# Kernel tuning notes

Measured on AMD Instinct MI355X. Metric: run time of the kernel, lower is better.

## Reference

```python
import jax, jax.numpy as jnp
import numpy as np

D = 1024
H = 16
DH = D // H
L = 128  # max_pos_len
B = 4
T = 1024
SCALE = float(np.sqrt(D / H))


def setup_inputs() -> dict:
    key = jax.random.key(0)
    ks = jax.random.split(key, 9)
    x_q = jax.random.normal(ks[0], (B, T, D), dtype=jnp.float32)
    x_k = jax.random.normal(ks[1], (B, T, D), dtype=jnp.float32)
    x_v = jax.random.normal(ks[2], (B, T, D), dtype=jnp.float32)
    mask = jax.random.randint(ks[3], (B, 1, 1, T), 0, 2) == 1  # bool, True = masked
    Wq = jax.random.normal(ks[4], (D, D), dtype=jnp.float32) * 0.02
    Wk = jax.random.normal(ks[5], (D, D), dtype=jnp.float32) * 0.02
    Wv = jax.random.normal(ks[6], (D, D), dtype=jnp.float32) * 0.02
    Wo = jax.random.normal(ks[7], (D, D), dtype=jnp.float32) * 0.02
    pos_emb = jax.random.normal(ks[8], (2 * L + 1, DH), dtype=jnp.float32)
    return {"x_q": x_q, "x_k": x_k, "x_v": x_v, "mask": mask,
            "Wq": Wq, "Wk": Wk, "Wv": Wv, "Wo": Wo, "pos_emb": pos_emb}


def reference(x_q, x_k, x_v, mask, Wq, Wk, Wv, Wo, pos_emb):
    # nn.Linear(bias=False): y = x @ W.T
    def split_heads(x):  # (B,T,D) -> (B,H,T,DH)
        return x.reshape(B, -1, H, DH).transpose(0, 2, 1, 3)

    Q = split_heads(x_q @ Wq.T)
    K = split_heads(x_k @ Wk.T)
    V = split_heads(x_v @ Wv.T)

    logits = jnp.einsum('bhqd,bhkd->bhqk', Q, K)

    # arrange_char_pos_embedding: indices[q,k] = clamp(k-q, -L, L) + L
    rel = jnp.clip(jnp.arange(T)[None, :] - jnp.arange(T)[:, None], -L, L) + L
    arranged_pos = pos_emb[rel]  # (T_Q, T_K, DH)
    pos_logits = jnp.einsum('bhqd,qkd->bhqk', Q, arranged_pos)

    logits = (logits + pos_logits) / SCALE
    logits = jnp.where(mask, -jnp.inf, logits)  # mask broadcasts (B,1,1,T)
    attn = jax.nn.softmax(logits, axis=-1)  # dropout p=0.0 -> identity

    combined = jnp.einsum('bhqk,bhkd->bhqd', attn, V)
    heads_concat = combined.transpose(0, 2, 1, 3).reshape(B, -1, D)
    return heads_concat @ Wo.T
```

## Files before the change

kernel.cpp:

```cpp
#include <hip/hip_runtime.h>
#include <hip/hip_bf16.h>
#include <stdint.h>

typedef __attribute__((ext_vector_type(8))) short short8;
typedef __attribute__((ext_vector_type(4))) float f32x4;

__device__ __forceinline__ uint16_t f2bf(float f) {
    union { float f; uint32_t u; } v; v.f = f;
    uint32_t r = v.u + 0x7FFF + ((v.u >> 16) & 1);
    return (uint16_t)(r >> 16);
}
__device__ __forceinline__ float bf2f(uint16_t u) {
    union { uint32_t u; float f; } v; v.u = ((uint32_t)u) << 16;
    return v.f;
}

template<int F32>
__device__ __forceinline__ uint4 load8(const void* p, size_t off) {
    if (F32) {
        const float* f = (const float*)p + off;
        float4 f0 = *(const float4*)f;
        float4 f1 = *(const float4*)(f + 4);
        uint4 r;
        r.x = (uint32_t)f2bf(f0.x) | ((uint32_t)f2bf(f0.y) << 16);
        r.y = (uint32_t)f2bf(f0.z) | ((uint32_t)f2bf(f0.w) << 16);
        r.z = (uint32_t)f2bf(f1.x) | ((uint32_t)f2bf(f1.y) << 16);
        r.w = (uint32_t)f2bf(f1.z) | ((uint32_t)f2bf(f1.w) << 16);
        return r;
    } else {
        return *(const uint4*)((const uint16_t*)p + off);
    }
}

#define GLDS(gp, lp) __builtin_amdgcn_global_load_lds( \
    (const __attribute__((address_space(1))) void*)(gp), \
    (__attribute__((address_space(3))) void*)(lp), 16, 0, 0)

struct CvtSeg { const float* s; uint16_t* d; int n8; };
struct CvtArgs { CvtSeg seg[9]; int nseg; const void* mraw; int* mcanon; };

__global__ __launch_bounds__(256) void cvt_bf16(CvtArgs a)
{
    if (blockIdx.x == 0) {
        __shared__ int flags[3];
        const uint32_t* w = (const uint32_t*)a.mraw;
        const uint8_t* b8 = (const uint8_t*)a.mraw;
        const int t = threadIdx.x;
        if (t < 3) flags[t] = 0;
        __syncthreads();
        int fbyte = 0, ff32 = 0, fodd = 0;
        for (int i = t; i < 1024; i += 256) {
            uint32_t v = w[i];
            if (v != 0u && v != 1u && v != 0x3F800000u) fbyte = 1;
            if (v == 0x3F800000u) ff32 = 1;
            if ((i & 1) && v != 0u) fodd = 1;
        }
        if (fbyte) atomicOr(&flags[0], 1);
        if (ff32)  atomicOr(&flags[1], 1);
        if (fodd)  atomicOr(&flags[2], 1);
        __syncthreads();
        int mode;
        if (flags[0]) mode = 1;
        else if (flags[1]) mode = 0;
        else if (!flags[2]) mode = 2;
        else mode = 0;
        for (int k = t; k < 4096; k += 256) {
            int val;
            if (mode == 1)      val = (b8[k] != 0);
            else if (mode == 2) val = (w[2 * k] != 0u);
            else                val = (w[k] != 0u);
            a.mcanon[k] = val;
        }
    }
    const int tid = blockIdx.x * 256 + threadIdx.x;
    const int stride = gridDim.x * 256;
    for (int s = 0; s < a.nseg; ++s) {
        const float* src = a.seg[s].s;
        uint16_t* dst = a.seg[s].d;
        const int n8 = a.seg[s].n8;
        if (src) {
            for (int i = tid; i < n8; i += stride)
                *(uint4*)(dst + (size_t)i * 8) = load8<1>(src, (size_t)i * 8);
        } else {
            const uint4 z = {0u, 0u, 0u, 0u};
            for (int i = tid; i < n8; i += stride)
                *(uint4*)(dst + (size_t)i * 8) = z;
        }
    }
}

__global__ __launch_bounds__(256) void gemm128_qkv(
    const uint16_t* __restrict__ xq, const uint16_t* __restrict__ xk, const uint16_t* __restrict__ xv,
    const uint16_t* __restrict__ Wq, const uint16_t* __restrict__ Wk, const uint16_t* __restrict__ Wv,
    uint16_t* __restrict__ Qh, uint16_t* __restrict__ Khd, uint16_t* __restrict__ Vt)
{
    __shared__ alignas(16) uint16_t As[2][128 * 32];
    __shared__ alignas(16) uint16_t Bs[2][128 * 32];

    const int z = blockIdx.z;
    const uint16_t* A = (z == 0) ? xq : (z == 1) ? xk : xv;
    const uint16_t* B = (z == 0) ? Wq : (z == 1) ? Wk : Wv;
    uint16_t* C = (z == 0) ? Qh : (z == 1) ? Khd : Vt;
    const int cm = (z == 2) ? 2 : 1;
    const int bm = blockIdx.x, bn = blockIdx.y;
    const int K = 1024;

    const int t = threadIdx.x;
    const int lane = t & 63, wave = t >> 6;
    const int lrow = lane & 15, quad = lane >> 4;
    const int wr = (wave >> 1) * 64, wc = (wave & 1) * 64;
    const int g_row = wave * 16 + (lane >> 2);
    const int g_col = (lane & 3) * 8;

    const f32x4 fz = {0.f, 0.f, 0.f, 0.f};
    f32x4 acc[4][4];
#pragma unroll
    for (int i = 0; i < 4; ++i)
#pragma unroll
        for (int j = 0; j < 4; ++j) acc[i][j] = fz;

    for (int k0 = 0; k0 < K; k0 += 64) {
        __syncthreads();
#pragma unroll
        for (int kh = 0; kh < 2; ++kh) {
            const int kk = k0 + kh * 32;
            GLDS(A + (size_t)(bm * 128 + g_row) * K + kk + g_col,      As[kh] + wave * 512);
            GLDS(A + (size_t)(bm * 128 + g_row + 64) * K + kk + g_col, As[kh] + wave * 512 + 2048);
            GLDS(B + (size_t)(bn * 128 + g_row) * K + kk + g_col,      Bs[kh] + wave * 512);
            GLDS(B + (size_t)(bn * 128 + g_row + 64) * K + kk + g_col, Bs[kh] + wave * 512 + 2048);
        }
        __syncthreads();

#pragma unroll
        for (int kh = 0; kh < 2; ++kh) {
            short8 a[4], b[4];
#pragma unroll
            for (int i = 0; i < 4; ++i)
                a[i] = *(const short8*)(As[kh] + (wr + i * 16 + lrow) * 32 + quad * 8);
#pragma unroll
            for (int j = 0; j < 4; ++j)
                b[j] = *(const short8*)(Bs[kh] + (wc + j * 16 + lrow) * 32 + quad * 8);
#pragma unroll
            for (int i = 0; i < 4; ++i)
#pragma unroll
                for (int j = 0; j < 4; ++j)
                    acc[i][j] = __builtin_amdgcn_mfma_f32_16x16x32_bf16(a[i], b[j], acc[i][j], 0, 0, 0);
        }
    }

    if (cm == 2) {
        __syncthreads();
        uint16_t* scr = As[0] + wave * 1024;
#pragma unroll
        for (int i = 0; i < 4; ++i)
#pragma unroll
            for (int j = 0; j < 4; ++j) {
                uint2 pk;
                pk.x = (uint32_t)f2bf(acc[i][j][0]) | ((uint32_t)f2bf(acc[i][j][1]) << 16);
                pk.y = (uint32_t)f2bf(acc[i][j][2]) | ((uint32_t)f2bf(acc[i][j][3]) << 16);
                *(uint2*)(scr + lrow * 16 + quad * 4) = pk;
                if (lane < 32) {
                    int n = lane >> 1, m8 = (lane & 1) * 8;
                    short8 vv = *(const short8*)(scr + n * 16 + m8);
                    int ng = bn * 128 + wc + j * 16 + n;
                    int hh = ng >> 6, d = ng & 63;
                    int mg = bm * 128 + wr + i * 16;
                    int bb = mg >> 10, tl = (mg & 1023) + m8;
                    *(short8*)(C + ((((size_t)bb * 16 + hh) * 64 + d) * 1024 + tl)) = vv;
                }
            }
        return;
    }

#pragma unroll
    for (int i = 0; i < 4; ++i)
#pragma unroll
        for (int j = 0; j < 4; ++j)
#pragma unroll
            for (int r = 0; r < 4; ++r) {
                int m = bm * 128 + wr + i * 16 + quad * 4 + r;
                int n = bn * 128 + wc + j * 16 + lrow;
                int bb = m >> 10, tt = m & 1023, hh = n >> 6, d = n & 63;
                C[(((size_t)bb * 16 + hh) * 1024 + tt) * 64 + d] = f2bf(acc[i][j][r]);
            }
}

__global__ __launch_bounds__(256) void gemm_out(
    const uint16_t* __restrict__ A, const uint16_t* __restrict__ B,
    float* __restrict__ C, int M, int N, int K)
{
    __shared__ alignas(16) uint16_t As[2][64 * 32];
    __shared__ alignas(16) uint16_t Bs[2][128 * 32];

    const int t = threadIdx.x;
    const int lane = t & 63, wave = t >> 6;
    const int lrow = lane & 15, quad = lane >> 4;
    const int wr = (wave >> 1) * 32, wc = (wave & 1) * 64;
    const int g_row = wave * 16 + (lane >> 2);
    const int g_col = (lane & 3) * 8;
    const int bm = blockIdx.x, bn = blockIdx.y;

    const f32x4 fz = {0.f, 0.f, 0.f, 0.f};
    f32x4 acc[2][4];
#pragma unroll
    for (int i = 0; i < 2; ++i)
#pragma unroll
        for (int j = 0; j < 4; ++j) acc[i][j] = fz;

    for (int k0 = 0; k0 < K; k0 += 64) {
        __syncthreads();
#pragma unroll
        for (int kh = 0; kh < 2; ++kh) {
            const int kk = k0 + kh * 32;
            GLDS(A + (size_t)(bm * 64 + g_row) * K + kk + g_col,       As[kh] + wave * 512);
            GLDS(B + (size_t)(bn * 128 + g_row) * K + kk + g_col,      Bs[kh] + wave * 512);
            GLDS(B + (size_t)(bn * 128 + g_row + 64) * K + kk + g_col, Bs[kh] + wave * 512 + 2048);
        }
        __syncthreads();

#pragma unroll
        for (int kh = 0; kh < 2; ++kh) {
            short8 a[2], b[4];
#pragma unroll
            for (int i = 0; i < 2; ++i)
                a[i] = *(const short8*)(As[kh] + (wr + i * 16 + lrow) * 32 + quad * 8);
#pragma unroll
            for (int j = 0; j < 4; ++j)
                b[j] = *(const short8*)(Bs[kh] + (wc + j * 16 + lrow) * 32 + quad * 8);
#pragma unroll
            for (int i = 0; i < 2; ++i)
#pragma unroll
                for (int j = 0; j < 4; ++j)
                    acc[i][j] = __builtin_amdgcn_mfma_f32_16x16x32_bf16(a[i], b[j], acc[i][j], 0, 0, 0);
        }
    }

#pragma unroll
    for (int i = 0; i < 2; ++i)
#pragma unroll
        for (int j = 0; j < 4; ++j)
#pragma unroll
            for (int r = 0; r < 4; ++r) {
                int m = bm * 64 + wr + i * 16 + quad * 4 + r;
                int n = bn * 128 + wc + j * 16 + lrow;
                C[(size_t)m * N + n] = acc[i][j][r];
            }
}

__global__ __launch_bounds__(256) void flash_attn(
    const uint16_t* __restrict__ Qh, const uint16_t* __restrict__ Kh,
    const uint16_t* __restrict__ Vt, const uint16_t* __restrict__ pos,
    const int* __restrict__ mask, uint16_t* __restrict__ comb)
{
    const int blk = blockIdx.x;
    const int jj = blk >> 3;
    const int bh = (blk & 7) * 8 + (jj >> 4);
    const int qt = jj & 15;
    const int b = bh >> 4;
    const int h = bh & 15;
    const int t = threadIdx.x;
    const int lane = t & 63;
    const int wave = t >> 6;
    const int lrow = lane & 15;
    const int quad = lane >> 4;
    const int qb = qt * 64 + wave * 16;

    __shared__ alignas(16) uint16_t Ks[2][4096];
    __shared__ alignas(16) uint16_t Vs[2][4096];
    __shared__ alignas(16) uint16_t Qpos_l[64][274];
    __shared__ alignas(16) uint16_t Pl[4][16][72];

    const uint16_t* Kp = Kh + (size_t)bh * 65536;
    const uint16_t* Vp = Vt + (size_t)bh * 65536;
    const int* mk = mask + b * 1024;

    const int sg_r = lane >> 2;
    const int sg_c = (lane & 3) * 8;
    const int hw = wave >> 1;
    const int gw = (wave & 1) * 2;

#pragma unroll
    for (int gg = 0; gg < 2; ++gg) {
        int g = gw + gg;
        GLDS(Kp + (size_t)(g * 16 + sg_r) * 64 + hw * 32 + sg_c, &Ks[0][hw * 2048 + g * 512]);
        GLDS(Vp + (size_t)(g * 16 + sg_r) * 1024 + hw * 32 + sg_c, &Vs[0][hw * 2048 + g * 512]);
    }

    const uint16_t* Qp = Qh + ((size_t)bh * 1024 + qb) * 64;
    short8 aq0 = *(const short8*)(Qp + (size_t)lrow * 64 + quad * 8);
    short8 aq1 = *(const short8*)(Qp + (size_t)lrow * 64 + 32 + quad * 8);

    const f32x4 fz = {0.f, 0.f, 0.f, 0.f};

#pragma unroll 4
    for (int nt = 0; nt < 17; ++nt) {
        short8 pb0 = *(const short8*)(pos + (size_t)(nt * 16 + lrow) * 64 + quad * 8);
        short8 pb1 = *(const short8*)(pos + (size_t)(nt * 16 + lrow) * 64 + 32 + quad * 8);
        f32x4 c = __builtin_amdgcn_mfma_f32_16x16x32_bf16(aq0, pb0, fz, 0, 0, 0);
        c = __builtin_amdgcn_mfma_f32_16x16x32_bf16(aq1, pb1, c, 0, 0, 0);
#pragma unroll
        for (int r = 0; r < 4; ++r)
            Qpos_l[wave * 16 + quad * 4 + r][nt * 16 + lrow] = f2bf(c[r]);
    }

    float pcl[4], pch[4];
#pragma unroll
    for (int r = 0; r < 4; ++r) {
        int ql = wave * 16 + quad * 4 + r;
        pcl[r] = bf2f(Qpos_l[ql][0])   * 0.125f;
        pch[r] = bf2f(Qpos_l[ql][256]) * 0.125f;
    }

    f32x4 o[4] = {fz, fz, fz, fz};
    float lsum[4] = {0.f, 0.f, 0.f, 0.f};

    for (int kb = 0; kb < 1024; kb += 64) {
        const int cur = (kb >> 6) & 1;
        __syncthreads();
        if (kb + 64 < 1024) {
            const int nxt = cur ^ 1;
#pragma unroll
            for (int gg = 0; gg < 2; ++gg) {
                int g = gw + gg;
                GLDS(Kp + (size_t)(kb + 64 + g * 16 + sg_r) * 64 + hw * 32 + sg_c,
                     &Ks[nxt][hw * 2048 + g * 512]);
                GLDS(Vp + (size_t)(g * 16 + sg_r) * 1024 + kb + 64 + hw * 32 + sg_c,
                     &Vs[nxt][hw * 2048 + g * 512]);
            }
        }
        const uint16_t* Kc = Ks[cur];
        const uint16_t* Vc = Vs[cur];

        f32x4 s[4];
#pragma unroll
        for (int j = 0; j < 4; ++j) {
            short8 k0 = *(const short8*)(Kc + (j * 16 + lrow) * 32 + quad * 8);
            short8 k1 = *(const short8*)(Kc + 2048 + (j * 16 + lrow) * 32 + quad * 8);
            s[j] = __builtin_amdgcn_mfma_f32_16x16x32_bf16(aq0, k0, fz, 0, 0, 0);
            s[j] = __builtin_amdgcn_mfma_f32_16x16x32_bf16(aq1, k1, s[j], 0, 0, 0);
        }

        const int diff = kb - qb;
        if (diff <= -192 || diff >= 144) {
            const bool low = (diff <= -192);
#pragma unroll
            for (int j = 0; j < 4; ++j) {
                const int key = kb + j * 16 + lrow;
                const bool m = (mk[key] != 0);
#pragma unroll
                for (int r = 0; r < 4; ++r) {
                    float pc = low ? pcl[r] : pch[r];
                    float e = m ? 0.f : __expf(__builtin_fmaf(s[j][r], 0.125f, pc));
                    lsum[r] += e;
                    Pl[wave][quad * 4 + r][j * 16 + lrow] = f2bf(e);
                }
            }
        } else {
#pragma unroll
            for (int j = 0; j < 4; ++j) {
                const int key = kb + j * 16 + lrow;
                const bool m = (mk[key] != 0);
#pragma unroll
                for (int r = 0; r < 4; ++r) {
                    int q = qb + quad * 4 + r;
                    int ql = q & 63;
                    int rel = min(max(key - q, -128), 128) + 128;
                    float p = bf2f(Qpos_l[ql][rel]);
                    float e = m ? 0.f : __expf((s[j][r] + p) * 0.125f);
                    lsum[r] += e;
                    Pl[wave][quad * 4 + r][j * 16 + lrow] = f2bf(e);
                }
            }
        }
        short8 ap0 = *(const short8*)(&Pl[wave][lrow][quad * 8]);
        short8 ap1 = *(const short8*)(&Pl[wave][lrow][32 + quad * 8]);

#pragma unroll
        for (int dt = 0; dt < 4; ++dt) {
            short8 v0 = *(const short8*)(Vc + (dt * 16 + lrow) * 32 + quad * 8);
            short8 v1 = *(const short8*)(Vc + 2048 + (dt * 16 + lrow) * 32 + quad * 8);
            o[dt] = __builtin_amdgcn_mfma_f32_16x16x32_bf16(ap0, v0, o[dt], 0, 0, 0);
            o[dt] = __builtin_amdgcn_mfma_f32_16x16x32_bf16(ap1, v1, o[dt], 0, 0, 0);
        }
    }

#pragma unroll
    for (int off = 1; off < 16; off <<= 1)
#pragma unroll
        for (int r = 0; r < 4; ++r)
            lsum[r] += __shfl_xor(lsum[r], off);

    float inv[4];
#pragma unroll
    for (int r = 0; r < 4; ++r) inv[r] = 1.0f / lsum[r];

#pragma unroll
    for (int dt = 0; dt < 4; ++dt)
#pragma unroll
        for (int r = 0; r < 4; ++r) {
            size_t row = (size_t)b * 1024 + qb + quad * 4 + r;
            size_t col = (size_t)h * 64 + dt * 16 + lrow;
            comb[row * 1024 + col] = f2bf(o[dt][r] * inv[r]);
        }
}

extern "C" void kernel_launch(void* const* d_in, const int* in_sizes, int n_in,
                              void* d_out, int out_size, void* d_ws, size_t ws_size,
                              hipStream_t stream)
{
    const float* x_q = (const float*)d_in[0];
    const float* x_k = (const float*)d_in[1];
    const float* x_v = (const float*)d_in[2];
    const void*  msk = d_in[3];
    const float* Wq  = (const float*)d_in[4];
    const float* Wk  = (const float*)d_in[5];
    const float* Wv  = (const float*)d_in[6];
    const float* Wo  = (const float*)d_in[7];
    const float* pos = (const float*)d_in[8];

    char* ws = (char*)d_ws;
    const size_t MB = 1u << 20;
    uint16_t* Qh   = (uint16_t*)(ws);
    uint16_t* Khd  = (uint16_t*)(ws + 8 * MB);
    uint16_t* Vt   = (uint16_t*)(ws + 16 * MB);
    uint16_t* xqb  = (uint16_t*)(ws + 24 * MB);
    uint16_t* xkb  = (uint16_t*)(ws + 32 * MB);
    uint16_t* xvb  = (uint16_t*)(ws + 40 * MB);
    uint16_t* Wqb  = (uint16_t*)(ws + 48 * MB);
    uint16_t* Wkb  = (uint16_t*)(ws + 50 * MB);
    uint16_t* Wvb  = (uint16_t*)(ws + 52 * MB);
    uint16_t* Wob  = (uint16_t*)(ws + 54 * MB);
    uint16_t* posb = (uint16_t*)(ws + 56 * MB);
    int*      canon = (int*)(ws + 56 * MB + 65536);
    uint16_t* comb = xqb;

    CvtArgs ca{};
    int ns = 0;
    ca.seg[ns++] = {x_q, xqb, 524288};
    ca.seg[ns++] = {x_k, xkb, 524288};
    ca.seg[ns++] = {x_v, xvb, 524288};
    ca.seg[ns++] = {Wq, Wqb, 131072};
    ca.seg[ns++] = {Wk, Wkb, 131072};
    ca.seg[ns++] = {Wv, Wvb, 131072};
    ca.seg[ns++] = {Wo, Wob, 131072};
    ca.seg[ns++] = {pos, posb, 2056};
    ca.seg[ns++] = {nullptr, posb + 16448, 120};
    ca.nseg = ns;
    ca.mraw = msk;
    ca.mcanon = canon;
    cvt_bf16<<<dim3(512), dim3(256), 0, stream>>>(ca);

    gemm128_qkv<<<dim3(32, 8, 3), dim3(256), 0, stream>>>(
        xqb, xkb, xvb, Wqb, Wkb, Wvb, Qh, Khd, Vt);

    flash_attn<<<dim3(1024), dim3(256), 0, stream>>>(Qh, Khd, Vt, posb, canon, comb);

    gemm_out<<<dim3(64, 8), dim3(256), 0, stream>>>(
        comb, Wob, (float*)d_out, 4096, 1024, 1024);
}
```

Before: 245.8 us.

## Bitpack mask, swizzle K/V LDS, use exp2 and packed bf16 converts in attention

Packs the attention mask into 64-bit words so each key tile reads one word instead of per-key int loads. Applies an XOR swizzle to the K/V LDS layout to cut bank conflicts, and pads Qpos rows differently. Folds the 1/8 scale and log2(e) into a single constant so the raw hardware exp2 replaces expf, and uses packed bf16 conversion instructions. It also raises wave priority around the MFMA blocks. The raw exp2 and pre-scaled bf16 position logits slightly change rounding.

```diff
diff --git a/kernel.cpp b/kernel.cpp
--- a/kernel.cpp
+++ b/kernel.cpp
@@ -13,6 +13,16 @@
 __device__ __forceinline__ float bf2f(uint16_t u) {
     union { uint32_t u; float f; } v; v.u = ((uint32_t)u) << 16;
     return v.f;
+}
+__device__ __forceinline__ float exp2_raw(float x) {
+    float r;
+    asm("v_exp_f32 %0, %1" : "=v"(r) : "v"(x));
+    return r;
+}
+__device__ __forceinline__ uint32_t cvt_pk_bf16(float lo, float hi) {
+    uint32_t r;
+    asm("v_cvt_pk_bf16_f32 %0, %1, %2" : "=v"(r) : "v"(lo), "v"(hi));
+    return r;
 }
 
 template<int F32>
@@ -37,12 +47,13 @@
     (__attribute__((address_space(3))) void*)(lp), 16, 0, 0)
 
 struct CvtSeg { const float* s; uint16_t* d; int n8; };
-struct CvtArgs { CvtSeg seg[9]; int nseg; const void* mraw; int* mcanon; };
+struct CvtArgs { CvtSeg seg[9]; int nseg; const void* mraw; unsigned long long* mbits; };
 
 __global__ __launch_bounds__(256) void cvt_bf16(CvtArgs a)
 {
     if (blockIdx.x == 0) {
         __shared__ int flags[3];
+        __shared__ uint8_t mloc[4096];
         const uint32_t* w = (const uint32_t*)a.mraw;
         const uint8_t* b8 = (const uint8_t*)a.mraw;
         const int t = threadIdx.x;
@@ -69,7 +80,15 @@
             if (mode == 1)      val = (b8[k] != 0);
             else if (mode == 2) val = (w[2 * k] != 0u);
             else                val = (w[k] != 0u);
-            a.mcanon[k] = val;
+            mloc[k] = (uint8_t)val;
+        }
+        __syncthreads();
+        if (t < 64) {
+            uint64_t bits = 0;
+#pragma unroll
+            for (int i = 0; i < 64; ++i)
+                bits |= (uint64_t)mloc[t * 64 + i] << i;
+            a.mbits[t] = bits;
         }
     }
     const int tid = blockIdx.x * 256 + threadIdx.x;
@@ -250,7 +269,7 @@
 __global__ __launch_bounds__(256) void flash_attn(
     const uint16_t* __restrict__ Qh, const uint16_t* __restrict__ Kh,
     const uint16_t* __restrict__ Vt, const uint16_t* __restrict__ pos,
-    const int* __restrict__ mask, uint16_t* __restrict__ comb)
+    const unsigned long long* __restrict__ mask64, uint16_t* __restrict__ comb)
 {
     const int blk = blockIdx.x;
     const int jj = blk >> 3;
@@ -267,17 +286,20 @@
 
     __shared__ alignas(16) uint16_t Ks[2][4096];
     __shared__ alignas(16) uint16_t Vs[2][4096];
-    __shared__ alignas(16) uint16_t Qpos_l[64][274];
+    __shared__ alignas(16) uint16_t Qpos_l[64][277];
     __shared__ alignas(16) uint16_t Pl[4][16][72];
 
     const uint16_t* Kp = Kh + (size_t)bh * 65536;
     const uint16_t* Vp = Vt + (size_t)bh * 65536;
-    const int* mk = mask + b * 1024;
+    const unsigned long long* mk64 = mask64 + b * 16;
 
     const int sg_r = lane >> 2;
-    const int sg_c = (lane & 3) * 8;
+    const int sg_c = ((lane & 3) ^ ((sg_r >> 1) & 3)) * 8;
     const int hw = wave >> 1;
     const int gw = (wave & 1) * 2;
+    const int rdc = (quad ^ ((lrow >> 1) & 3)) * 8;
+
+    const float CS = 0.18033688011f;
 
 #pragma unroll
     for (int gg = 0; gg < 2; ++gg) {
@@ -298,17 +320,22 @@
         short8 pb1 = *(const short8*)(pos + (size_t)(nt * 16 + lrow) * 64 + 32 + quad * 8);
         f32x4 c = __builtin_amdgcn_mfma_f32_16x16x32_bf16(aq0, pb0, fz, 0, 0, 0);
         c = __builtin_amdgcn_mfma_f32_16x16x32_bf16(aq1, pb1, c, 0, 0, 0);
-#pragma unroll
-        for (int r = 0; r < 4; ++r)
-            Qpos_l[wave * 16 + quad * 4 + r][nt * 16 + lrow] = f2bf(c[r]);
+        const uint32_t p01 = cvt_pk_bf16(c[0] * CS, c[1] * CS);
+        const uint32_t p23 = cvt_pk_bf16(c[2] * CS, c[3] * CS);
+        const int row = wave * 16 + quad * 4;
+        const int col = nt * 16 + lrow;
+        Qpos_l[row + 0][col] = (uint16_t)p01;
+        Qpos_l[row + 1][col] = (uint16_t)(p01 >> 16);
+        Qpos_l[row + 2][col] = (uint16_t)p23;
+        Qpos_l[row + 3][col] = (uint16_t)(p23 >> 16);
     }
 
     float pcl[4], pch[4];
 #pragma unroll
     for (int r = 0; r < 4; ++r) {
         int ql = wave * 16 + quad * 4 + r;
-        pcl[r] = bf2f(Qpos_l[ql][0])   * 0.125f;
-        pch[r] = bf2f(Qpos_l[ql][256]) * 0.125f;
+        pcl[r] = bf2f(Qpos_l[ql][0]);
+        pch[r] = bf2f(Qpos_l[ql][256]);
     }
 
     f32x4 o[4] = {fz, fz, fz, fz};
@@ -330,58 +357,82 @@
         }
         const uint16_t* Kc = Ks[cur];
         const uint16_t* Vc = Vs[cur];
+        const unsigned long long mb = mk64[kb >> 6];
 
         f32x4 s[4];
+        __builtin_amdgcn_s_setprio(1);
 #pragma unroll
         for (int j = 0; j < 4; ++j) {
-            short8 k0 = *(const short8*)(Kc + (j * 16 + lrow) * 32 + quad * 8);
-            short8 k1 = *(const short8*)(Kc + 2048 + (j * 16 + lrow) * 32 + quad * 8);
+            short8 k0 = *(const short8*)(Kc + (j * 16 + lrow) * 32 + rdc);
+            short8 k1 = *(const short8*)(Kc + 2048 + (j * 16 + lrow) * 32 + rdc);
             s[j] = __builtin_amdgcn_mfma_f32_16x16x32_bf16(aq0, k0, fz, 0, 0, 0);
             s[j] = __builtin_amdgcn_mfma_f32_16x16x32_bf16(aq1, k1, s[j], 0, 0, 0);
         }
+        __builtin_amdgcn_s_setprio(0);
 
         const int diff = kb - qb;
         if (diff <= -192 || diff >= 144) {
             const bool low = (diff <= -192);
 #pragma unroll
             for (int j = 0; j < 4; ++j) {
-                const int key = kb + j * 16 + lrow;
-                const bool m = (mk[key] != 0);
+                const uint32_t mj = ((uint32_t)(mb >> (j * 16)) >> lrow) & 1u;
+                float e[4];
 #pragma unroll
                 for (int r = 0; r < 4; ++r) {
                     float pc = low ? pcl[r] : pch[r];
-                    float e = m ? 0.f : __expf(__builtin_fmaf(s[j][r], 0.125f, pc));
-                    lsum[r] += e;
-                    Pl[wave][quad * 4 + r][j * 16 + lrow] = f2bf(e);
+                    float ev = exp2_raw(__builtin_fmaf(s[j][r], CS, pc));
+                    ev = mj ? 0.f : ev;
+                    lsum[r] += ev;
+                    e[r] = ev;
                 }
+                const uint32_t p01 = cvt_pk_bf16(e[0], e[1]);
+                const uint32_t p23 = cvt_pk_bf16(e[2], e[3]);
+                const int col = j * 16 + lrow;
+                const int rw = quad * 4;
+                Pl[wave][rw + 0][col] = (uint16_t)p01;
+                Pl[wave][rw + 1][col] = (uint16_t)(p01 >> 16);
+                Pl[wave][rw + 2][col] = (uint16_t)p23;
+                Pl[wave][rw + 3][col] = (uint16_t)(p23 >> 16);
             }
         } else {
 #pragma unroll
             for (int j = 0; j < 4; ++j) {
                 const int key = kb + j * 16 + lrow;
-                const bool m = (mk[key] != 0);
+                const uint32_t mj = ((uint32_t)(mb >> (j * 16)) >> lrow) & 1u;
+                float e[4];
 #pragma unroll
                 for (int r = 0; r < 4; ++r) {
                     int q = qb + quad * 4 + r;
                     int ql = q & 63;
                     int rel = min(max(key - q, -128), 128) + 128;
                     float p = bf2f(Qpos_l[ql][rel]);
-                    float e = m ? 0.f : __expf((s[j][r] + p) * 0.125f);
-                    lsum[r] += e;
-                    Pl[wave][quad * 4 + r][j * 16 + lrow] = f2bf(e);
+                    float ev = exp2_raw(__builtin_fmaf(s[j][r], CS, p));
+                    ev = mj ? 0.f : ev;
+                    lsum[r] += ev;
+                    e[r] = ev;
                 }
+                const uint32_t p01 = cvt_pk_bf16(e[0], e[1]);
+                const uint32_t p23 = cvt_pk_bf16(e[2], e[3]);
+                const int col = j * 16 + lrow;
+                const int rw = quad * 4;
+                Pl[wave][rw + 0][col] = (uint16_t)p01;
+                Pl[wave][rw + 1][col] = (uint16_t)(p01 >> 16);
+                Pl[wave][rw + 2][col] = (uint16_t)p23;
+                Pl[wave][rw + 3][col] = (uint16_t)(p23 >> 16);
             }
         }
         short8 ap0 = *(const short8*)(&Pl[wave][lrow][quad * 8]);
         short8 ap1 = *(const short8*)(&Pl[wave][lrow][32 + quad * 8]);
 
+        __builtin_amdgcn_s_setprio(1);
 #pragma unroll
         for (int dt = 0; dt < 4; ++dt) {
-            short8 v0 = *(const short8*)(Vc + (dt * 16 + lrow) * 32 + quad * 8);
-            short8 v1 = *(const short8*)(Vc + 2048 + (dt * 16 + lrow) * 32 + quad * 8);
+            short8 v0 = *(const short8*)(Vc + (dt * 16 + lrow) * 32 + rdc);
+            short8 v1 = *(const short8*)(Vc + 2048 + (dt * 16 + lrow) * 32 + rdc);
             o[dt] = __builtin_amdgcn_mfma_f32_16x16x32_bf16(ap0, v0, o[dt], 0, 0, 0);
             o[dt] = __builtin_amdgcn_mfma_f32_16x16x32_bf16(ap1, v1, o[dt], 0, 0, 0);
         }
+        __builtin_amdgcn_s_setprio(0);
     }
 
 #pragma unroll
@@ -431,7 +482,7 @@
     uint16_t* Wvb  = (uint16_t*)(ws + 52 * MB);
     uint16_t* Wob  = (uint16_t*)(ws + 54 * MB);
     uint16_t* posb = (uint16_t*)(ws + 56 * MB);
-    int*      canon = (int*)(ws + 56 * MB + 65536);
+    unsigned long long* mbits = (unsigned long long*)(ws + 56 * MB + 65536);
     uint16_t* comb = xqb;
 
     CvtArgs ca{};
@@ -447,13 +498,13 @@
     ca.seg[ns++] = {nullptr, posb + 16448, 120};
     ca.nseg = ns;
     ca.mraw = msk;
-    ca.mcanon = canon;
+    ca.mbits = mbits;
     cvt_bf16<<<dim3(512), dim3(256), 0, stream>>>(ca);
 
     gemm128_qkv<<<dim3(32, 8, 3), dim3(256), 0, stream>>>(
         xqb, xkb, xvb, Wqb, Wkb, Wvb, Qh, Khd, Vt);
 
-    flash_attn<<<dim3(1024), dim3(256), 0, stream>>>(Qh, Khd, Vt, posb, canon, comb);
+    flash_attn<<<dim3(1024), dim3(256), 0, stream>>>(Qh, Khd, Vt, posb, mbits, comb);
 
     gemm_out<<<dim3(64, 8), dim3(256), 0, stream>>>(
         comb, Wob, (float*)d_out, 4096, 1024, 1024);
```

Result: faster. 230.0 us (-6.4%).
